# Optimization experiments

Measured on AMD Instinct MI355X. Metric: run time of the kernel, lower is better.

## Reference

```python
import jax, jax.numpy as jnp
import numpy as np

VOCAB, EMB, HID, LABELS, NUM_LAYERS = 32000, 512, 1024, 64, 2
B, S = 32, 512


def setup_inputs() -> dict:
    key = jax.random.key(0)
    ks = jax.random.split(key, 12)
    s_e = 1.0 / np.sqrt(EMB)
    s_h = 1.0 / np.sqrt(HID)
    inp = {
        "tokens": jax.random.randint(ks[0], (B, S), 0, VOCAB),
        "emb": jax.random.normal(ks[1], (VOCAB, EMB), jnp.float32),
        # layer 0: input dim EMB
        "W_ih0": jax.random.uniform(ks[2], (HID, EMB), jnp.float32, -s_h, s_h),
        "W_hh0": jax.random.uniform(ks[3], (HID, HID), jnp.float32, -s_h, s_h),
        "b_ih0": jax.random.uniform(ks[4], (HID,), jnp.float32, -s_h, s_h),
        "b_hh0": jax.random.uniform(ks[5], (HID,), jnp.float32, -s_h, s_h),
        # layer 1: input dim HID
        "W_ih1": jax.random.uniform(ks[6], (HID, HID), jnp.float32, -s_h, s_h),
        "W_hh1": jax.random.uniform(ks[7], (HID, HID), jnp.float32, -s_h, s_h),
        "b_ih1": jax.random.uniform(ks[8], (HID,), jnp.float32, -s_h, s_h),
        "b_hh1": jax.random.uniform(ks[9], (HID,), jnp.float32, -s_h, s_h),
        "W_out": jax.random.uniform(ks[10], (LABELS, HID), jnp.float32, -s_h, s_h),
        "b_out": jax.random.uniform(ks[11], (LABELS,), jnp.float32, -s_h, s_h),
    }
    return inp


def _rnn_layer(x, W_ih, W_hh, b_ih, b_hh):
    # x: [B,S,in] -> h_t = tanh(W_ih x_t + b_ih + W_hh h_{t-1} + b_hh)
    # Precompute input projection for all timesteps (one big GEMM).
    xp = jnp.einsum('bsi,hi->bsh', x, W_ih) + (b_ih + b_hh)  # [B,S,H]
    h0 = jnp.zeros((x.shape[0], W_hh.shape[0]), x.dtype)

    def step(h, xt):
        h = jnp.tanh(xt + h @ W_hh.T)
        return h, h

    _, ys = jax.lax.scan(step, h0, jnp.swapaxes(xp, 0, 1))  # [S,B,H]
    return jnp.swapaxes(ys, 0, 1)  # [B,S,H]


def reference(tokens, emb, W_ih0, W_hh0, b_ih0, b_hh0,
              W_ih1, W_hh1, b_ih1, b_hh1, W_out, b_out):
    x = emb[tokens]  # [B,S,EMB]
    h = _rnn_layer(x, W_ih0, W_hh0, b_ih0, b_hh0)
    h = _rnn_layer(h, W_ih1, W_hh1, b_ih1, b_hh1)
    return jnp.einsum('bsh,lh->bsl', h, W_out) + b_out  # [B,S,LABELS]
```

## Files before the change

kernel.cpp:

```cpp
#include <hip/hip_runtime.h>
#include <math.h>

#define B_    32
#define S_    512
#define EMB_  512
#define HID_  1024
#define LAB_  64
#define M_    (B_ * S_)

#define SLOT_U64   2048
#define LS_STRIDE  (8 * SLOT_U64)
#define EX_TOTAL   (2 * 4 * LS_STRIDE)
#define EPMASK64   0x4000000040000000ULL
#define NANPAT64   0x7FC000007FC00000ULL
#define ONEPAT64   0x3F8000003F800000ULL
#define PAYMASK    0xBFFFFFFFu

__device__ __forceinline__ unsigned long long aload64(const unsigned long long* p) {
    return __hip_atomic_load((unsigned long long*)p, __ATOMIC_RELAXED,
                             __HIP_MEMORY_SCOPE_AGENT);
}
__device__ __forceinline__ void astore64(unsigned long long* p, unsigned long long v) {
    __hip_atomic_store(p, v, __ATOMIC_RELAXED, __HIP_MEMORY_SCOPE_AGENT);
}
__device__ __forceinline__ float2 exdec(unsigned long long u) {
    return make_float2(__uint_as_float((unsigned)u & PAYMASK),
                       __uint_as_float((unsigned)(u >> 32) & PAYMASK));
}
__device__ __forceinline__ float fold16(float* v, int kg) {
#pragma unroll
    for (int st = 0; st < 4; ++st) {
        const int m  = 1 << st;
        const int nh = 8 >> st;
        const bool hi = (kg & m) != 0;
#pragma unroll
        for (int j = 0; j < 8; ++j) {
            if (j < nh) {
                const float a0 = v[2*j], a1 = v[2*j+1];
                const float got = __shfl_xor(hi ? a0 : a1, m, 64);
                v[j] = (hi ? a1 : a0) + got;
            }
        }
    }
    float r = v[0];
    r += __shfl_xor(r, 16, 64);
    r += __shfl_xor(r, 32, 64);
    return r;
}

__global__ __launch_bounds__(256) void gemm_bias(
    const float* __restrict__ A, const int* __restrict__ tokens,
    const float* __restrict__ W, const float* __restrict__ bias,
    const float* __restrict__ bias2, float* __restrict__ C,
    int M, int K, int N)
{
    __shared__ float As[128][17];
    __shared__ float Ws[64][17];

    const int tid = threadIdx.x;
    const int tx  = tid & 15;
    const int ty  = tid >> 4;
    const int n0  = blockIdx.x * 64;
    const int m0  = blockIdx.y * 128;

    const int lr  = tid >> 2;
    const int lk  = (tid & 3) << 2;

    const int ar0 = tokens ? tokens[m0 + lr]      : (m0 + lr);
    const int ar1 = tokens ? tokens[m0 + 64 + lr] : (m0 + 64 + lr);
    const float* __restrict__ arow0 = A + (size_t)ar0 * K;
    const float* __restrict__ arow1 = A + (size_t)ar1 * K;
    const float* __restrict__ wrow  = W + (size_t)(n0 + lr) * K;

    float bs[4];
#pragma unroll
    for (int j = 0; j < 4; ++j) {
        int n = n0 + tx * 4 + j;
        bs[j] = bias[n] + (bias2 ? bias2[n] : 0.0f);
    }

    float acc[8][4] = {};

    for (int k0 = 0; k0 < K; k0 += 16) {
        const float4 a0 = *(const float4*)(arow0 + k0 + lk);
        const float4 a1 = *(const float4*)(arow1 + k0 + lk);
        const float4 wv = *(const float4*)(wrow  + k0 + lk);
        __syncthreads();
        As[lr][lk + 0] = a0.x; As[lr][lk + 1] = a0.y;
        As[lr][lk + 2] = a0.z; As[lr][lk + 3] = a0.w;
        As[64 + lr][lk + 0] = a1.x; As[64 + lr][lk + 1] = a1.y;
        As[64 + lr][lk + 2] = a1.z; As[64 + lr][lk + 3] = a1.w;
        Ws[lr][lk + 0] = wv.x; Ws[lr][lk + 1] = wv.y;
        Ws[lr][lk + 2] = wv.z; Ws[lr][lk + 3] = wv.w;
        __syncthreads();

#pragma unroll
        for (int kk = 0; kk < 16; ++kk) {
            float b[4], a[8];
#pragma unroll
            for (int j = 0; j < 4; ++j) b[j] = Ws[tx * 4 + j][kk];
#pragma unroll
            for (int i = 0; i < 8; ++i) a[i] = As[ty * 8 + i][kk];
#pragma unroll
            for (int i = 0; i < 8; ++i)
#pragma unroll
                for (int j = 0; j < 4; ++j)
                    acc[i][j] += a[i] * b[j];
        }
    }

#pragma unroll
    for (int i = 0; i < 8; ++i) {
        const int m = m0 + ty * 8 + i;
        float4 v;
        v.x = acc[i][0] + bs[0];
        v.y = acc[i][1] + bs[1];
        v.z = acc[i][2] + bs[2];
        v.w = acc[i][3] + bs[3];
        *(float4*)(C + (size_t)m * N + n0 + tx * 4) = v;
    }
}

__global__ __launch_bounds__(256) void fill_poison(unsigned long long* p, int n)
{
    const int i = blockIdx.x * 256 + threadIdx.x;
    if (i < n) {
        const int ls = i / LS_STRIDE;
        p[i] = (ls == 4) ? ONEPAT64 : NANPAT64;
    }
}

__global__ __launch_bounds__(512, 2) void rnn_fused(
    const float* __restrict__ Whh0, const float* __restrict__ Whh1,
    const float* __restrict__ Wih1, const float* __restrict__ b_ih1,
    const float* __restrict__ b_hh1, float* __restrict__ xb,
    unsigned long long* __restrict__ ex)
{
    extern __shared__ float smem[];
    float2* hb = (float2*)smem;

    const int wg  = blockIdx.x;
    const int g   = wg & 7;
    const int s   = wg >> 3;
    const int tid = threadIdx.x;
    const int j8  = tid >> 6;
    const int kg  = tid & 63;
    const int b0  = g * 4;

    float w0[4][16], wx[4][16], wh[4][16];
    {
        const size_t base = (size_t)(s * 32 + j8 * 4) * HID_ + kg;
#pragma unroll
        for (int i = 0; i < 4; ++i)
#pragma unroll
            for (int q = 0; q < 16; ++q) {
                const size_t o = base + (size_t)i * HID_ + (size_t)q * 64;
                w0[i][q] = Whh0[o];
                wx[i][q] = Wih1[o];
                wh[i][q] = Whh1[o];
            }
    }

    const int i4 = (kg >> 2) & 3;
    const int bb = kg & 3;
    const int ok = s * 32 + j8 * 4 + i4;
    float bsum = 0.f;
    if (kg < 16) bsum = b_ih1[ok] + b_hh1[ok];

    float* px0 = xb + ((size_t)(b0 + bb) * S_) * HID_ + ok;
    float* px1 = px0;

    unsigned long long* const exg = ex + (size_t)g * SLOT_U64;

    for (int r = 0; r <= S_; ++r) {
        float xpv = 0.f;
        if (kg < 16 && r < S_) xpv = *px0;
        px0 += HID_;

        const int cur = r & 1;
        float2* s0 = hb + (size_t)cur * 2048;
        float2* s1 = hb + (size_t)(2 + cur) * 2048;

        if (r == 0) {
#pragma unroll
            for (int k = 0; k < 4; ++k) {
                s0[tid + 512 * k] = make_float2(0.f, 0.f);
                s1[tid + 512 * k] = make_float2(0.f, 0.f);
            }
        } else {
            const int sl = (r - 1) & 3;
            const unsigned long long want =
                (((unsigned)(r - 1) >> 2) & 1u) ? EPMASK64 : 0ULL;
            const unsigned long long* pl0 = exg + (size_t)sl * LS_STRIDE;
            const unsigned long long* pl1 = exg + (size_t)(4 + sl) * LS_STRIDE;
            unsigned pend = (r >= 2) ? 0xFFu : 0x0Fu;
            if (r == 1) {
#pragma unroll
                for (int k = 0; k < 4; ++k)
                    s1[tid + 512 * k] = make_float2(0.f, 0.f);
            }
            do {
#pragma unroll
                for (int k = 0; k < 4; ++k) {
                    if (pend & (1u << k)) {
                        const unsigned long long u = aload64(pl0 + tid + 512 * k);
                        if ((u & EPMASK64) == want) {
                            s0[tid + 512 * k] = exdec(u);
                            pend &= ~(1u << k);
                        }
                    }
                    if (pend & (1u << (4 + k))) {
                        const unsigned long long u = aload64(pl1 + tid + 512 * k);
                        if ((u & EPMASK64) == want) {
                            s1[tid + 512 * k] = exdec(u);
                            pend &= ~(1u << (4 + k));
                        }
                    }
                }
            } while (pend);
        }
        __syncthreads();

        {
            float v[16] = {};
#pragma unroll
            for (int q = 0; q < 16; ++q) {
                const float2 a0 = s0[q * 64 + kg];
                const float2 a1 = s0[1024 + q * 64 + kg];
#pragma unroll
                for (int i = 0; i < 4; ++i) {
                    const float fa = w0[i][q];
                    v[i*4+0] += fa * a0.x; v[i*4+1] += fa * a0.y;
                    v[i*4+2] += fa * a1.x; v[i*4+3] += fa * a1.y;
                }
            }
            const float r0 = fold16(v, kg);
            if (r < S_) {
                float h0 = 0.f;
                if (kg < 16) h0 = tanhf(xpv + r0);
                const float h0p = __shfl_xor(h0, 1, 64);
                if (kg < 16 && (bb & 1) == 0) {
                    const unsigned eb = (((unsigned)r >> 2) & 1u) << 30;
                    const unsigned long long u =
                        ((unsigned long long)(__float_as_uint(h0p) | eb) << 32) |
                        (unsigned long long)(__float_as_uint(h0) | eb);
                    astore64(exg + (size_t)(r & 3) * LS_STRIDE
                                 + ((size_t)(bb >> 1) << 10) + ok, u);
                }
            }
        }

        if (r >= 1) {
            float v[16] = {};
#pragma unroll
            for (int q = 0; q < 16; ++q) {
                const float2 a0 = s0[q * 64 + kg];
                const float2 a1 = s0[1024 + q * 64 + kg];
                const float2 c0 = s1[q * 64 + kg];
                const float2 c1 = s1[1024 + q * 64 + kg];
#pragma unroll
                for (int i = 0; i < 4; ++i) {
                    const float fb = wx[i][q];
                    v[i*4+0] += fb * a0.x; v[i*4+1] += fb * a0.y;
                    v[i*4+2] += fb * a1.x; v[i*4+3] += fb * a1.y;
                    const float fc = wh[i][q];
                    v[i*4+0] += fc * c0.x; v[i*4+1] += fc * c0.y;
                    v[i*4+2] += fc * c1.x; v[i*4+3] += fc * c1.y;
                }
            }
            const float r1 = fold16(v, kg);
            float h1 = 0.f;
            if (kg < 16) h1 = tanhf(r1 + bsum);
            const float h1p = __shfl_xor(h1, 1, 64);
            if (kg < 16) *px1 = h1;
            if (kg < 16 && (bb & 1) == 0) {
                const unsigned eb = (((unsigned)r >> 2) & 1u) << 30;
                const unsigned long long u =
                    ((unsigned long long)(__float_as_uint(h1p) | eb) << 32) |
                    (unsigned long long)(__float_as_uint(h1) | eb);
                astore64(exg + (size_t)(4 + (r & 3)) * LS_STRIDE
                             + ((size_t)(bb >> 1) << 10) + ok, u);
            }
            px1 += HID_;
        }
    }
}

extern "C" void kernel_launch(void* const* d_in, const int* in_sizes, int n_in,
                              void* d_out, int out_size, void* d_ws, size_t ws_size,
                              hipStream_t stream)
{
    const int*   tokens = (const int*)  d_in[0];
    const float* emb    = (const float*)d_in[1];
    const float* W_ih0  = (const float*)d_in[2];
    const float* W_hh0  = (const float*)d_in[3];
    const float* b_ih0  = (const float*)d_in[4];
    const float* b_hh0  = (const float*)d_in[5];
    const float* W_ih1  = (const float*)d_in[6];
    const float* W_hh1  = (const float*)d_in[7];
    const float* b_ih1  = (const float*)d_in[8];
    const float* b_hh1  = (const float*)d_in[9];
    const float* W_out  = (const float*)d_in[10];
    const float* b_out  = (const float*)d_in[11];
    float* out = (float*)d_out;

    float* buf = (float*)d_ws;
    unsigned long long* ex = (unsigned long long*)d_out;

    const size_t scan_lds = 98304;
    hipFuncSetAttribute((const void*)rnn_fused,
                        hipFuncAttributeMaxDynamicSharedMemorySize, (int)scan_lds);

    gemm_bias<<<dim3(HID_ / 64, M_ / 128), 256, 0, stream>>>(
        emb, tokens, W_ih0, b_ih0, b_hh0, buf, M_, EMB_, HID_);

    fill_poison<<<EX_TOTAL / 256, 256, 0, stream>>>(ex, EX_TOTAL);

    rnn_fused<<<256, 512, scan_lds, stream>>>(
        W_hh0, W_hh1, W_ih1, b_ih1, b_hh1, buf, ex);

    gemm_bias<<<dim3(LAB_ / 64, M_ / 128), 256, 0, stream>>>(
        buf, nullptr, W_out, b_out, nullptr, out, M_, HID_, LAB_);
}
```

Before: 3.675 ms.

## Split layer exchange polls and use 128-bit interleaved flag loads

Stores in the inter-block hidden-state exchange buffer are interleaved so each thread can poll two 128-bit chunks with inline-asm dwordx4 loads, replacing eight 64-bit atomic loads per step. The layer-1 recurrent-state wait is moved after the layer-0 compute, with an extra barrier, so layer-0 work overlaps the wait for other blocks' layer-1 outputs. This is meant to cut polling latency and serialization on the critical path. In exchange it relies on 128-bit loads being untorn with respect to the 64-bit stores, since each epoch bit is checked per dword, and it adds one barrier per step.

```diff
diff --git a/kernel.cpp b/kernel.cpp
--- a/kernel.cpp
+++ b/kernel.cpp
@@ -11,21 +11,30 @@
 #define SLOT_U64   2048
 #define LS_STRIDE  (8 * SLOT_U64)
 #define EX_TOTAL   (2 * 4 * LS_STRIDE)
-#define EPMASK64   0x4000000040000000ULL
+#define EPBIT      0x40000000u
 #define NANPAT64   0x7FC000007FC00000ULL
 #define ONEPAT64   0x3F8000003F800000ULL
 #define PAYMASK    0xBFFFFFFFu
 
-__device__ __forceinline__ unsigned long long aload64(const unsigned long long* p) {
-    return __hip_atomic_load((unsigned long long*)p, __ATOMIC_RELAXED,
-                             __HIP_MEMORY_SCOPE_AGENT);
-}
+typedef unsigned int u32x4 __attribute__((ext_vector_type(4)));
+
 __device__ __forceinline__ void astore64(unsigned long long* p, unsigned long long v) {
     __hip_atomic_store(p, v, __ATOMIC_RELAXED, __HIP_MEMORY_SCOPE_AGENT);
 }
-__device__ __forceinline__ float2 exdec(unsigned long long u) {
-    return make_float2(__uint_as_float((unsigned)u & PAYMASK),
-                       __uint_as_float((unsigned)(u >> 32) & PAYMASK));
+__device__ __forceinline__ void apoll2(const unsigned long long* q0,
+                                       const unsigned long long* q1,
+                                       u32x4& w0, u32x4& w1) {
+    asm volatile(
+        "global_load_dwordx4 %0, %2, off sc1\n\t"
+        "global_load_dwordx4 %1, %3, off sc1\n\t"
+        "s_waitcnt vmcnt(0)"
+        : "=&v"(w0), "=&v"(w1)
+        : "v"(q0), "v"(q1)
+        : "memory");
+}
+__device__ __forceinline__ bool epok4(u32x4 v, unsigned eb) {
+    return ((((v[0] ^ eb) | (v[1] ^ eb)) | ((v[2] ^ eb) | (v[3] ^ eb)))
+            & EPBIT) == 0;
 }
 __device__ __forceinline__ float fold16(float* v, int kg) {
 #pragma unroll
@@ -171,6 +180,7 @@
     float* px1 = px0;
 
     unsigned long long* const exg = ex + (size_t)g * SLOT_U64;
+    const int c0 = 2 * tid, c1 = 1024 + 2 * tid;
 
     for (int r = 0; r <= S_; ++r) {
         float xpv = 0.f;
@@ -181,41 +191,36 @@
         float2* s0 = hb + (size_t)cur * 2048;
         float2* s1 = hb + (size_t)(2 + cur) * 2048;
 
+        const int sl = (r - 1) & 3;
+        const unsigned eb = ((((unsigned)(r - 1)) >> 2) & 1u) << 30;
+
         if (r == 0) {
 #pragma unroll
-            for (int k = 0; k < 4; ++k) {
+            for (int k = 0; k < 4; ++k)
                 s0[tid + 512 * k] = make_float2(0.f, 0.f);
-                s1[tid + 512 * k] = make_float2(0.f, 0.f);
-            }
         } else {
-            const int sl = (r - 1) & 3;
-            const unsigned long long want =
-                (((unsigned)(r - 1) >> 2) & 1u) ? EPMASK64 : 0ULL;
-            const unsigned long long* pl0 = exg + (size_t)sl * LS_STRIDE;
-            const unsigned long long* pl1 = exg + (size_t)(4 + sl) * LS_STRIDE;
-            unsigned pend = (r >= 2) ? 0xFFu : 0x0Fu;
-            if (r == 1) {
-#pragma unroll
-                for (int k = 0; k < 4; ++k)
-                    s1[tid + 512 * k] = make_float2(0.f, 0.f);
-            }
+            const unsigned long long* pl = exg + (size_t)sl * LS_STRIDE;
+            unsigned pend = 3u;
+            u32x4 w0v, w1v;
             do {
-#pragma unroll
-                for (int k = 0; k < 4; ++k) {
-                    if (pend & (1u << k)) {
-                        const unsigned long long u = aload64(pl0 + tid + 512 * k);
-                        if ((u & EPMASK64) == want) {
-                            s0[tid + 512 * k] = exdec(u);
-                            pend &= ~(1u << k);
-                        }
-                    }
-                    if (pend & (1u << (4 + k))) {
-                        const unsigned long long u = aload64(pl1 + tid + 512 * k);
-                        if ((u & EPMASK64) == want) {
-                            s1[tid + 512 * k] = exdec(u);
-                            pend &= ~(1u << (4 + k));
-                        }
-                    }
+                apoll2(pl + c0, pl + c1, w0v, w1v);
+                if ((pend & 1u) && epok4(w0v, eb)) {
+                    s0[tid]        = make_float2(
+                        __uint_as_float(w0v[0] & PAYMASK),
+                        __uint_as_float(w0v[1] & PAYMASK));
+                    s0[1024 + tid] = make_float2(
+                        __uint_as_float(w0v[2] & PAYMASK),
+                        __uint_as_float(w0v[3] & PAYMASK));
+                    pend &= ~1u;
+                }
+                if ((pend & 2u) && epok4(w1v, eb)) {
+                    s0[512 + tid]  = make_float2(
+                        __uint_as_float(w1v[0] & PAYMASK),
+                        __uint_as_float(w1v[1] & PAYMASK));
+                    s0[1536 + tid] = make_float2(
+                        __uint_as_float(w1v[2] & PAYMASK),
+                        __uint_as_float(w1v[3] & PAYMASK));
+                    pend &= ~2u;
                 }
             } while (pend);
         }
@@ -240,15 +245,47 @@
                 if (kg < 16) h0 = tanhf(xpv + r0);
                 const float h0p = __shfl_xor(h0, 1, 64);
                 if (kg < 16 && (bb & 1) == 0) {
-                    const unsigned eb = (((unsigned)r >> 2) & 1u) << 30;
+                    const unsigned pe = (((unsigned)r >> 2) & 1u) << 30;
                     const unsigned long long u =
-                        ((unsigned long long)(__float_as_uint(h0p) | eb) << 32) |
-                        (unsigned long long)(__float_as_uint(h0) | eb);
+                        ((unsigned long long)(__float_as_uint(h0p) | pe) << 32) |
+                        (unsigned long long)(__float_as_uint(h0) | pe);
                     astore64(exg + (size_t)(r & 3) * LS_STRIDE
-                                 + ((size_t)(bb >> 1) << 10) + ok, u);
-                }
-            }
-        }
+                                 + 2 * ok + (bb >> 1), u);
+                }
+            }
+        }
+
+        if (r == 1) {
+#pragma unroll
+            for (int k = 0; k < 4; ++k)
+                s1[tid + 512 * k] = make_float2(0.f, 0.f);
+        } else if (r >= 2) {
+            const unsigned long long* pl = exg + (size_t)(4 + sl) * LS_STRIDE;
+            unsigned pend = 3u;
+            u32x4 w0v, w1v;
+            do {
+                apoll2(pl + c0, pl + c1, w0v, w1v);
+                if ((pend & 1u) && epok4(w0v, eb)) {
+                    s1[tid]        = make_float2(
+                        __uint_as_float(w0v[0] & PAYMASK),
+                        __uint_as_float(w0v[1] & PAYMASK));
+                    s1[1024 + tid] = make_float2(
+                        __uint_as_float(w0v[2] & PAYMASK),
+                        __uint_as_float(w0v[3] & PAYMASK));
+                    pend &= ~1u;
+                }
+                if ((pend & 2u) && epok4(w1v, eb)) {
+                    s1[512 + tid]  = make_float2(
+                        __uint_as_float(w1v[0] & PAYMASK),
+                        __uint_as_float(w1v[1] & PAYMASK));
+                    s1[1536 + tid] = make_float2(
+                        __uint_as_float(w1v[2] & PAYMASK),
+                        __uint_as_float(w1v[3] & PAYMASK));
+                    pend &= ~2u;
+                }
+            } while (pend);
+        }
+        __syncthreads();
 
         if (r >= 1) {
             float v[16] = {};
@@ -256,16 +293,16 @@
             for (int q = 0; q < 16; ++q) {
                 const float2 a0 = s0[q * 64 + kg];
                 const float2 a1 = s0[1024 + q * 64 + kg];
-                const float2 c0 = s1[q * 64 + kg];
-                const float2 c1 = s1[1024 + q * 64 + kg];
+                const float2 c0f = s1[q * 64 + kg];
+                const float2 c1f = s1[1024 + q * 64 + kg];
 #pragma unroll
                 for (int i = 0; i < 4; ++i) {
                     const float fb = wx[i][q];
                     v[i*4+0] += fb * a0.x; v[i*4+1] += fb * a0.y;
                     v[i*4+2] += fb * a1.x; v[i*4+3] += fb * a1.y;
                     const float fc = wh[i][q];
-                    v[i*4+0] += fc * c0.x; v[i*4+1] += fc * c0.y;
-                    v[i*4+2] += fc * c1.x; v[i*4+3] += fc * c1.y;
+                    v[i*4+0] += fc * c0f.x; v[i*4+1] += fc * c0f.y;
+                    v[i*4+2] += fc * c1f.x; v[i*4+3] += fc * c1f.y;
                 }
             }
             const float r1 = fold16(v, kg);
@@ -274,12 +311,12 @@
             const float h1p = __shfl_xor(h1, 1, 64);
             if (kg < 16) *px1 = h1;
             if (kg < 16 && (bb & 1) == 0) {
-                const unsigned eb = (((unsigned)r >> 2) & 1u) << 30;
+                const unsigned pe = (((unsigned)r >> 2) & 1u) << 30;
                 const unsigned long long u =
-                    ((unsigned long long)(__float_as_uint(h1p) | eb) << 32) |
-                    (unsigned long long)(__float_as_uint(h1) | eb);
+                    ((unsigned long long)(__float_as_uint(h1p) | pe) << 32) |
+                    (unsigned long long)(__float_as_uint(h1) | pe);
                 astore64(exg + (size_t)(4 + (r & 3)) * LS_STRIDE
-                             + ((size_t)(bb >> 1) << 10) + ok, u);
+                             + 2 * ok + (bb >> 1), u);
             }
             px1 += HID_;
         }
```

After: 3.258 ms. 1.13x faster.
